# Optimization experiments

Hardware: AMD Instinct MI355X
Metric: run time of the kernel (lower is better)

The kernel has to match this reference:

```python
import jax, jax.numpy as jnp
import numpy as np

SIGMA = 100.0
M = 64
N_DIMS = 3
XH_IN = 9           # n_dims + in_node_nf + context_node_nf
XH_HID = 64         # xh_hidden_size
POS_HID = 192       # hidden_size - xh_hidden_size
TWO_PI = 2.0 * np.pi


def setup_inputs() -> dict:
    key = jax.random.key(0)
    ks = jax.random.split(key, 6)
    B, N = 8, 256
    t = jax.random.uniform(ks[0], (B, 1), dtype=jnp.float32)
    xh = jax.random.normal(ks[1], (B, N, XH_IN), dtype=jnp.float32)
    node_mask = jnp.ones((B, N, 1), dtype=jnp.float32)
    edge_mask = jnp.ones((B, N * N, 1), dtype=jnp.float32)
    # learned params: xh_embedder Linear(9->64), pos_embedder Linear(2m->192)
    W_xh = jax.random.normal(ks[2], (XH_IN, XH_HID), dtype=jnp.float32) / np.sqrt(XH_IN)
    b_xh = jnp.zeros((XH_HID,), dtype=jnp.float32)
    W_pos = jax.random.normal(ks[3], (2 * M, POS_HID), dtype=jnp.float32) / np.sqrt(2 * M)
    b_pos = jnp.zeros((POS_HID,), dtype=jnp.float32)
    return {"t": t, "xh": xh, "node_mask": node_mask, "edge_mask": edge_mask,
            "W_xh": W_xh, "b_xh": b_xh, "W_pos": W_pos, "b_pos": b_pos}


def remove_mean_with_mask(x, node_mask, N):
    # masked mean over node axis, re-masked output
    mean = jnp.sum(x * node_mask, axis=1, keepdims=True) / N  # [B,1,3]
    return (x - mean) * node_mask


def positional_encoding(d, sigma, m):
    # d: [B,N,N,1] -> Fourier features [B,N,N,2m] with geometric freqs sigma^(j/m)
    freqs = sigma ** (jnp.arange(m, dtype=jnp.float32) / m)  # [m]
    ang = TWO_PI * d * freqs                                  # [B,N,N,m]
    return jnp.concatenate([jnp.sin(ang), jnp.cos(ang)], axis=-1)


def reference(t, xh, node_mask, edge_mask, W_xh, b_xh, W_pos, b_pos):
    x = xh[..., :N_DIMS]
    h = xh[..., N_DIMS:]
    N = jnp.sum(node_mask, axis=1, keepdims=True)  # [B,1,1]
    x = remove_mean_with_mask(x, node_mask, N)
    # node feature embedding: [B,N,64]
    xh_emb = jnp.concatenate([x, h], axis=-1) @ W_xh + b_xh
    # pairwise distances (safe sqrt for diagonal zeros)
    diff = x[:, :, None, :] - x[:, None, :, :]                 # [B,N,N,3]
    sq = jnp.maximum(jnp.sum(diff * diff, axis=-1), 0.0)
    dist = jnp.sqrt(sq + 1e-12)                                # [B,N,N]
    pe = positional_encoding(dist[..., None], SIGMA, M)        # [B,N,N,2m]
    pe = pe * node_mask[:, :, :, None] * node_mask[:, None, :, :]
    pe = (pe @ W_pos + b_pos)                                  # [B,N,N,192]
    pe = jnp.sum(pe, axis=-2) / N                              # [B,N,192]
    out = jnp.concatenate([xh_emb, pe], axis=-1) * node_mask   # [B,N,256]
    return out
```

## Files before the change

### kernel.cpp

```cpp
#include <hip/hip_runtime.h>
#include <math.h>

#define BB 8
#define NN 256
#define XHIN 9
#define XHHID 64
#define POSHID 192

__global__ __launch_bounds__(256) void mean_kernel(
    const float* __restrict__ xh, const float* __restrict__ mask,
    float* __restrict__ ws_xc, float* __restrict__ ws_cnt)
{
  const int b = blockIdx.x;
  const int n = threadIdx.x;

  const float* p = xh + (b * NN + n) * XHIN;
  const float x0 = p[0], x1 = p[1], x2 = p[2];
  const float m = mask[b * NN + n];

  float a0 = x0 * m, a1 = x1 * m, a2 = x2 * m, a3 = m;
  #pragma unroll
  for (int off = 32; off > 0; off >>= 1) {
    a0 += __shfl_down(a0, off, 64);
    a1 += __shfl_down(a1, off, 64);
    a2 += __shfl_down(a2, off, 64);
    a3 += __shfl_down(a3, off, 64);
  }
  __shared__ float red[4][4];
  const int lane = n & 63, wv = n >> 6;
  if (lane == 0) { red[wv][0] = a0; red[wv][1] = a1; red[wv][2] = a2; red[wv][3] = a3; }
  __syncthreads();

  const float s0 = red[0][0] + red[1][0] + red[2][0] + red[3][0];
  const float s1 = red[0][1] + red[1][1] + red[2][1] + red[3][1];
  const float s2 = red[0][2] + red[1][2] + red[2][2] + red[3][2];
  const float cnt = red[0][3] + red[1][3] + red[2][3] + red[3][3];
  const float inv = 1.0f / cnt;

  ws_xc[(b * 3 + 0) * NN + n] = (x0 - s0 * inv) * m;
  ws_xc[(b * 3 + 1) * NN + n] = (x1 - s1 * inv) * m;
  ws_xc[(b * 3 + 2) * NN + n] = (x2 - s2 * inv) * m;
  if (n == 0) ws_cnt[b] = cnt;
}

__global__ __launch_bounds__(256) void pe_kernel(
    const float* __restrict__ ws_xc, const float* __restrict__ ws_cnt,
    const float* __restrict__ mask, const float* __restrict__ xh,
    const float* __restrict__ Wxh, const float* __restrict__ bxh,
    const float* __restrict__ Wp, const float* __restrict__ bp,
    float* __restrict__ out)
{
  const int blk = blockIdx.x;
  const int b = blk >> 8;
  const int i = blk & 255;
  const int tid = threadIdx.x;

  __shared__ float2 dm_s[NN];
  __shared__ float part[4][128];
  __shared__ __align__(16) float Ssc[128];
  __shared__ float ins_s[XHIN];

  const float* xcb = ws_xc + b * 3 * NN;
  const float xi0 = xcb[0 * NN + i];
  const float xi1 = xcb[1 * NN + i];
  const float xi2 = xcb[2 * NN + i];
  {
    const int j = tid;
    const float dx = xi0 - xcb[0 * NN + j];
    const float dy = xi1 - xcb[1 * NN + j];
    const float dz = xi2 - xcb[2 * NN + j];
    const float sq = fmaf(dx, dx, fmaf(dy, dy, dz * dz));
    dm_s[j] = make_float2(sqrtf(sq + 1e-12f), mask[b * NN + j]);
  }
  if (tid < XHIN)
    ins_s[tid] = (tid < 3) ? xcb[tid * NN + i] : xh[(b * NN + i) * XHIN + tid];
  __syncthreads();

  const int f = tid & 63, jg = tid >> 6;
  const float freq = __builtin_exp2f((float)f * 0.10381025296523007f);
  float ss = 0.f, cc = 0.f;
  const float2* dmp = dm_s + jg * 64;
  #pragma unroll 16
  for (int u = 0; u < 64; ++u) {
    const float2 dm = dmp[u];
    const float rv = __builtin_amdgcn_fractf(dm.x * freq);
    ss = fmaf(__builtin_amdgcn_sinf(rv), dm.y, ss);
    cc = fmaf(__builtin_amdgcn_cosf(rv), dm.y, cc);
  }
  part[jg][f] = ss;
  part[jg][64 + f] = cc;
  __syncthreads();

  const float cnt = ws_cnt[b];
  const float mi = dm_s[i].y;
  if (tid < 128)
    Ssc[tid] = (part[0][tid] + part[1][tid] + part[2][tid] + part[3][tid]) * (mi / cnt);
  __syncthreads();

  if (tid < POSHID) {
    const float4* S4 = (const float4*)Ssc;
    float acc = bp[tid] * (mi * 256.0f / cnt);
    #pragma unroll 8
    for (int k4 = 0; k4 < 32; ++k4) {
      const float4 s = S4[k4];
      const float* w = Wp + (k4 * 4) * POSHID + tid;
      acc = fmaf(s.x, w[0 * POSHID], acc);
      acc = fmaf(s.y, w[1 * POSHID], acc);
      acc = fmaf(s.z, w[2 * POSHID], acc);
      acc = fmaf(s.w, w[3 * POSHID], acc);
    }
    out[(size_t)(b * NN + i) * 256 + 64 + tid] = acc;
  } else {
    const int oo = tid - POSHID;
    float acc = bxh[oo];
    #pragma unroll
    for (int k = 0; k < XHIN; ++k)
      acc = fmaf(ins_s[k], Wxh[k * XHHID + oo], acc);
    out[(size_t)(b * NN + i) * 256 + oo] = acc * mi;
  }
}

extern "C" void kernel_launch(void* const* d_in, const int* in_sizes, int n_in,
                              void* d_out, int out_size, void* d_ws, size_t ws_size,
                              hipStream_t stream) {
  const float* xh   = (const float*)d_in[1];
  const float* mask = (const float*)d_in[2];
  const float* Wxh  = (const float*)d_in[4];
  const float* bxh  = (const float*)d_in[5];
  const float* Wp   = (const float*)d_in[6];
  const float* bp   = (const float*)d_in[7];
  float* out = (float*)d_out;

  float* ws_xc  = (float*)d_ws;
  float* ws_cnt = ws_xc + BB * 3 * NN;

  mean_kernel<<<BB, 256, 0, stream>>>(xh, mask, ws_xc, ws_cnt);
  pe_kernel<<<BB * NN, 256, 0, stream>>>(ws_xc, ws_cnt, mask, xh, Wxh, bxh, Wp, bp, out);
}
```

Before: 81.51 us.

## Split PE kernel into S-field pass and multi-row output GEMV kernel

The fused per-row kernel is split in two. The first kernel computes the masked sin/cos sums per row and writes them to workspace. A second kernel then does the 128x192 projection for 4 rows per block, so each W_pos load is reused across rows, and it also stages W_xh in shared memory. This cuts redundant weight traffic but adds a kernel launch and a round trip of the S buffer through global memory.

```diff
diff --git a/kernel.cpp b/kernel.cpp
--- a/kernel.cpp
+++ b/kernel.cpp
@@ -6,6 +6,7 @@
 #define XHIN 9
 #define XHHID 64
 #define POSHID 192
+#define RPB 4
 
 __global__ __launch_bounds__(256) void mean_kernel(
     const float* __restrict__ xh, const float* __restrict__ mask,
@@ -43,12 +44,9 @@
   if (n == 0) ws_cnt[b] = cnt;
 }
 
-__global__ __launch_bounds__(256) void pe_kernel(
+__global__ __launch_bounds__(256) void sfield_kernel(
     const float* __restrict__ ws_xc, const float* __restrict__ ws_cnt,
-    const float* __restrict__ mask, const float* __restrict__ xh,
-    const float* __restrict__ Wxh, const float* __restrict__ bxh,
-    const float* __restrict__ Wp, const float* __restrict__ bp,
-    float* __restrict__ out)
+    const float* __restrict__ mask, float* __restrict__ ws_S)
 {
   const int blk = blockIdx.x;
   const int b = blk >> 8;
@@ -57,8 +55,6 @@
 
   __shared__ float2 dm_s[NN];
   __shared__ float part[4][128];
-  __shared__ __align__(16) float Ssc[128];
-  __shared__ float ins_s[XHIN];
 
   const float* xcb = ws_xc + b * 3 * NN;
   const float xi0 = xcb[0 * NN + i];
@@ -72,8 +68,6 @@
     const float sq = fmaf(dx, dx, fmaf(dy, dy, dz * dz));
     dm_s[j] = make_float2(sqrtf(sq + 1e-12f), mask[b * NN + j]);
   }
-  if (tid < XHIN)
-    ins_s[tid] = (tid < 3) ? xcb[tid * NN + i] : xh[(b * NN + i) * XHIN + tid];
   __syncthreads();
 
   const int f = tid & 63, jg = tid >> 6;
@@ -91,32 +85,88 @@
   part[jg][64 + f] = cc;
   __syncthreads();
 
-  const float cnt = ws_cnt[b];
-  const float mi = dm_s[i].y;
+  if (tid < 128) {
+    const float cnt = ws_cnt[b];
+    const float mi = dm_s[i].y;
+    ws_S[(size_t)blk * 128 + tid] =
+        (part[0][tid] + part[1][tid] + part[2][tid] + part[3][tid]) * (mi / cnt);
+  }
+}
+
+__global__ __launch_bounds__(256) void out_kernel(
+    const float* __restrict__ ws_S, const float* __restrict__ ws_xc,
+    const float* __restrict__ ws_cnt, const float* __restrict__ mask,
+    const float* __restrict__ xh,
+    const float* __restrict__ Wxh, const float* __restrict__ bxh,
+    const float* __restrict__ Wp, const float* __restrict__ bp,
+    float* __restrict__ out)
+{
+  const int blk = blockIdx.x;
+  const int row0 = blk * RPB;
+  const int b = row0 >> 8;
+  const int i0 = row0 & 255;
+  const int tid = threadIdx.x;
+
+  __shared__ __align__(16) float S_l[RPB][128];
+  __shared__ float ins_l[RPB][XHIN];
+  __shared__ float Wxh_l[XHIN * XHHID];
+  __shared__ float bxh_l[XHHID];
+  __shared__ float bscale_l[RPB];
+  __shared__ float mi_l[RPB];
+
   if (tid < 128)
-    Ssc[tid] = (part[0][tid] + part[1][tid] + part[2][tid] + part[3][tid]) * (mi / cnt);
+    ((float4*)S_l)[tid] = ((const float4*)(ws_S + (size_t)row0 * 128))[tid];
+  if (tid < 192) {
+    Wxh_l[tid]       = Wxh[tid];
+    Wxh_l[tid + 192] = Wxh[tid + 192];
+    Wxh_l[tid + 384] = Wxh[tid + 384];
+  }
+  if (tid < XHHID) bxh_l[tid] = bxh[tid];
+  if (tid < RPB * XHIN) {
+    const int r = tid / XHIN, k = tid % XHIN;
+    const int i = i0 + r;
+    ins_l[r][k] = (k < 3) ? ws_xc[(b * 3 + k) * NN + i]
+                          : xh[(size_t)(b * NN + i) * XHIN + k];
+  }
+  if (tid < RPB) {
+    const float m = mask[b * NN + i0 + tid];
+    mi_l[tid] = m;
+    bscale_l[tid] = m * 256.0f / ws_cnt[b];
+  }
   __syncthreads();
 
   if (tid < POSHID) {
-    const float4* S4 = (const float4*)Ssc;
-    float acc = bp[tid] * (mi * 256.0f / cnt);
+    const int col = tid;
+    float acc[RPB];
+    #pragma unroll
+    for (int r = 0; r < RPB; ++r) acc[r] = bp[col] * bscale_l[r];
+
     #pragma unroll 8
     for (int k4 = 0; k4 < 32; ++k4) {
-      const float4 s = S4[k4];
-      const float* w = Wp + (k4 * 4) * POSHID + tid;
-      acc = fmaf(s.x, w[0 * POSHID], acc);
-      acc = fmaf(s.y, w[1 * POSHID], acc);
-      acc = fmaf(s.z, w[2 * POSHID], acc);
-      acc = fmaf(s.w, w[3 * POSHID], acc);
+      const float* w = Wp + (k4 * 4) * POSHID + col;
+      const float w0 = w[0 * POSHID];
+      const float w1 = w[1 * POSHID];
+      const float w2 = w[2 * POSHID];
+      const float w3 = w[3 * POSHID];
+      #pragma unroll
+      for (int r = 0; r < RPB; ++r) {
+        const float4 s = ((const float4*)S_l[r])[k4];
+        acc[r] = fmaf(s.w, w3, fmaf(s.z, w2, fmaf(s.y, w1, fmaf(s.x, w0, acc[r]))));
+      }
     }
-    out[(size_t)(b * NN + i) * 256 + 64 + tid] = acc;
+    #pragma unroll
+    for (int r = 0; r < RPB; ++r)
+      out[(size_t)(row0 + r) * 256 + 64 + col] = acc[r];
   } else {
     const int oo = tid - POSHID;
-    float acc = bxh[oo];
     #pragma unroll
-    for (int k = 0; k < XHIN; ++k)
-      acc = fmaf(ins_s[k], Wxh[k * XHHID + oo], acc);
-    out[(size_t)(b * NN + i) * 256 + oo] = acc * mi;
+    for (int r = 0; r < RPB; ++r) {
+      float acc = bxh_l[oo];
+      #pragma unroll
+      for (int k = 0; k < XHIN; ++k)
+        acc = fmaf(ins_l[r][k], Wxh_l[k * XHHID + oo], acc);
+      out[(size_t)(row0 + r) * 256 + oo] = acc * mi_l[r];
+    }
   }
 }
 
@@ -133,7 +183,10 @@
 
   float* ws_xc  = (float*)d_ws;
   float* ws_cnt = ws_xc + BB * 3 * NN;
+  float* ws_S   = ws_cnt + 64;
 
   mean_kernel<<<BB, 256, 0, stream>>>(xh, mask, ws_xc, ws_cnt);
-  pe_kernel<<<BB * NN, 256, 0, stream>>>(ws_xc, ws_cnt, mask, xh, Wxh, bxh, Wp, bp, out);
+  sfield_kernel<<<BB * NN, 256, 0, stream>>>(ws_xc, ws_cnt, mask, ws_S);
+  out_kernel<<<BB * NN / RPB, 256, 0, stream>>>(ws_S, ws_xc, ws_cnt, mask, xh,
+                                                Wxh, bxh, Wp, bp, out);
 }
```

Result: slower. 85.60 us (+5.0%).
